# Optimization experiments

Hardware: AMD Instinct MI355X
Metric: run time of the kernel (lower is better)

The kernel has to match this reference:

```python
import jax, jax.numpy as jnp
import numpy as np

BETA = 0.85
THR = 1.0
SLOPE = 25.0  # fast_sigmoid surrogate slope

@jax.custom_vjp
def spike_fn(v):
    # Heaviside fire with fast-sigmoid surrogate gradient (snntorch fast_sigmoid)
    return (v > 0).astype(v.dtype)

def _spike_fwd(v):
    return (v > 0).astype(v.dtype), v

def _spike_bwd(v, g):
    return (g / (SLOPE * jnp.abs(v) + 1.0) ** 2,)

spike_fn.defvjp(_spike_fwd, _spike_bwd)

def setup_inputs() -> dict:
    key = jax.random.key(0)
    k1, k2, k3, k4, k5 = jax.random.split(key, 5)
    B, T, IN, H = 32, 2048, 512, 256
    x = jax.random.normal(k1, (B, T, IN), dtype=jnp.float32)
    s_in = 1.0 / np.sqrt(IN)
    s_h = 1.0 / np.sqrt(H)
    W_in = jax.random.uniform(k2, (H, IN), jnp.float32, -s_in, s_in)
    b_in = jax.random.uniform(k3, (H,), jnp.float32, -s_in, s_in)
    V = jax.random.uniform(k4, (H, H), jnp.float32, -s_h, s_h)   # RLeaky recurrent linear
    b_rec = jax.random.uniform(k5, (H,), jnp.float32, -s_h, s_h)
    return {"x": x, "W_in": W_in, "b_in": b_in, "V": V, "b_rec": b_rec}

def reference(x, W_in, b_in, V, b_rec):
    B, T, _ = x.shape
    H = W_in.shape[0]
    # input projection for all timesteps at once: (B,T,H) -> (T,B,H)
    proj = jnp.einsum('bti,hi->bth', x, W_in) + b_in
    proj_t = jnp.transpose(proj, (1, 0, 2))

    def step(carry, p_t):
        spk, mem = carry
        input_ = p_t + spk                       # combined = proj[:,t] + spk
        rec = spk @ V.T + b_rec                   # RLeaky recurrent term
        reset = jax.lax.stop_gradient((mem > THR).astype(mem.dtype))
        mem = BETA * mem + input_ + rec - reset * THR  # subtract reset
        spk = spike_fn(mem - THR)
        return (spk, mem), spk

    init = (jnp.zeros((B, H), x.dtype), jnp.zeros((B, H), x.dtype))
    _, spikes = jax.lax.scan(step, init, proj_t)  # (T,B,H)
    return jnp.transpose(spikes, (1, 0, 2))       # (B,T,H)
```

## Files before the change

### kernel.cpp

```cpp
#include <hip/hip_runtime.h>
#include <cstddef>
#include <cstdint>

#define kB 32
#define kT 2048
#define kIn 512
#define kH 256
#define kBeta 0.85f
#define kThr 1.0f

#define N_SCAN kB
#define N_GEMM (kB * 8)
#define FLAGS_PER_B 8

#define GBM 256
#define GBK 16
#define GLDA 260

#define SSTRIDE 260
#define SM_PBUF 16
#define SM_PRING (SM_PBUF + 16 * SSTRIDE)
#define SM_OBUF  (SM_PRING + 16 * 256)
#define SMEM_SCAN (SM_OBUF + 8 * 256)
#define SMEM_GEMM (2 * GBK * GLDA)
#define SMEM_FLOATS (SMEM_SCAN > SMEM_GEMM ? SMEM_SCAN : SMEM_GEMM)

__device__ __forceinline__ void wait_flag(int* f) {
    while (__hip_atomic_load(f, __ATOMIC_ACQUIRE, __HIP_MEMORY_SCOPE_AGENT) == 0) {
        __builtin_amdgcn_s_sleep(2);
    }
}

__device__ __forceinline__ void scan_bar() {
    asm volatile("s_waitcnt lgkmcnt(0)" ::: "memory");
    __builtin_amdgcn_s_barrier();
}

__device__ void gemm_body(const float* __restrict__ A,
                          const float* __restrict__ W,
                          const float* __restrict__ bias,
                          float* __restrict__ P,
                          int* flags, int gid, float* smem)
{
    float* As = smem;
    float* Bs = smem + GBK * GLDA;
    const int tid = threadIdx.x;
    const int b  = gid & 31;
    const int tt = gid >> 5;
    const int bm = b * kT + tt * GBM;
    const int tx = tid & 31;
    const int ty = tid >> 5;

    float acc[8][8];
#pragma unroll
    for (int i = 0; i < 8; ++i)
#pragma unroll
        for (int j = 0; j < 8; ++j) acc[i][j] = 0.f;

    const int r = tid >> 2, kc = (tid & 3) << 2;

    for (int kb = 0; kb < kIn; kb += GBK) {
        const float4 av = *reinterpret_cast<const float4*>(A + (size_t)(bm + r) * kIn + kb + kc);
        const float4 bv = *reinterpret_cast<const float4*>(W + (size_t)r * kIn + kb + kc);
        __syncthreads();
        As[(kc + 0) * GLDA + r] = av.x;
        As[(kc + 1) * GLDA + r] = av.y;
        As[(kc + 2) * GLDA + r] = av.z;
        As[(kc + 3) * GLDA + r] = av.w;
        Bs[(kc + 0) * GLDA + r] = bv.x;
        Bs[(kc + 1) * GLDA + r] = bv.y;
        Bs[(kc + 2) * GLDA + r] = bv.z;
        Bs[(kc + 3) * GLDA + r] = bv.w;
        __syncthreads();

#pragma unroll
        for (int k = 0; k < GBK; ++k) {
            const float4 aa0 = *reinterpret_cast<const float4*>(&As[k * GLDA + ty * 4]);
            const float4 aa1 = *reinterpret_cast<const float4*>(&As[k * GLDA + ty * 4 + 128]);
            const float4 bb0 = *reinterpret_cast<const float4*>(&Bs[k * GLDA + tx * 4]);
            const float4 bb1 = *reinterpret_cast<const float4*>(&Bs[k * GLDA + tx * 4 + 128]);
            const float av8[8] = {aa0.x, aa0.y, aa0.z, aa0.w, aa1.x, aa1.y, aa1.z, aa1.w};
            const float bv8[8] = {bb0.x, bb0.y, bb0.z, bb0.w, bb1.x, bb1.y, bb1.z, bb1.w};
#pragma unroll
            for (int i = 0; i < 8; ++i)
#pragma unroll
                for (int j = 0; j < 8; ++j)
                    acc[i][j] = fmaf(av8[i], bv8[j], acc[i][j]);
        }
    }

    const float4 bl = *reinterpret_cast<const float4*>(bias + tx * 4);
    const float4 bh = *reinterpret_cast<const float4*>(bias + tx * 4 + 128);
#pragma unroll
    for (int i = 0; i < 8; ++i) {
        const int m = bm + ty * 4 + (i & 3) + ((i >> 2) << 7);
        float4 o0, o1;
        o0.x = acc[i][0] + bl.x; o0.y = acc[i][1] + bl.y;
        o0.z = acc[i][2] + bl.z; o0.w = acc[i][3] + bl.w;
        o1.x = acc[i][4] + bh.x; o1.y = acc[i][5] + bh.y;
        o1.z = acc[i][6] + bh.z; o1.w = acc[i][7] + bh.w;
        *reinterpret_cast<float4*>(P + (size_t)m * kH + tx * 4) = o0;
        *reinterpret_cast<float4*>(P + (size_t)m * kH + tx * 4 + 128) = o1;
    }

    __syncthreads();
    if (flags && tid == 0) {
        __threadfence();
        atomicAdd(flags + b * FLAGS_PER_B + tt, 1);
    }
}

__device__ void scan_body(float* __restrict__ PO,
                          const float* __restrict__ V,
                          const float* __restrict__ brec,
                          int* flags, float* smem)
{
    unsigned long long* smask = reinterpret_cast<unsigned long long*>(smem);
    float* pbuf  = smem + SM_PBUF;
    float* pring = smem + SM_PRING;
    float* obuf  = smem + SM_OBUF;

    const int b = blockIdx.x;
    const int tid = threadIdx.x;
    const int w = tid >> 6;
    const int l = tid & 63;
    const int h0 = l << 2;
    const int kc = w << 4;
    const bool owner = (tid < kH);
    const int h = tid & (kH - 1);

    float Vr[4][16];
#pragma unroll
    for (int i = 0; i < 4; ++i) {
        const float4* vp = reinterpret_cast<const float4*>(V + (size_t)(h0 + i) * kH + kc);
#pragma unroll
        for (int c4 = 0; c4 < 4; ++c4) {
            const float4 v = vp[c4];
            Vr[i][c4 * 4 + 0] = v.x; Vr[i][c4 * 4 + 1] = v.y;
            Vr[i][c4 * 4 + 2] = v.z; Vr[i][c4 * 4 + 3] = v.w;
        }
    }

    const float br = owner ? brec[h] : 0.f;
    float mem = 0.f, spk = 0.f;
    float* po_b = PO + (size_t)b * (size_t)kT * kH;

    if (tid < 4) smask[tid] = 0ull;

    int* bflags = flags ? (flags + b * FLAGS_PER_B) : nullptr;

    if (w == 15) {
        if (bflags) wait_flag(bflags + 0);
#pragma unroll
        for (int r = 0; r < 8; ++r) {
            const float4 v = *reinterpret_cast<const float4*>(po_b + (size_t)r * kH + 4 * l);
            *reinterpret_cast<float4*>(pring + r * 256 + 4 * l) = v;
        }
    }
    scan_bar();

    const int mshift = (w & 3) << 4;

    for (int tb = 0; tb < kT / 8; ++tb) {
        float4 g0, g1, g2, g3, g4, g5, g6, g7;
#pragma unroll
        for (int ti = 0; ti < 8; ++ti) {
            const int t = tb * 8 + ti;

            if (ti == 0) {
                if (w == 15 && tb < kT / 8 - 1) {
                    if (bflags && ((tb + 1) & 31) == 0 && ((tb + 1) >> 5) < 8)
                        wait_flag(bflags + ((tb + 1) >> 5));
                    const size_t r0 = (size_t)(tb * 8 + 8) * kH + 4 * l;
                    g0 = *reinterpret_cast<const float4*>(po_b + r0 + 0 * kH);
                    g1 = *reinterpret_cast<const float4*>(po_b + r0 + 1 * kH);
                    g2 = *reinterpret_cast<const float4*>(po_b + r0 + 2 * kH);
                    g3 = *reinterpret_cast<const float4*>(po_b + r0 + 3 * kH);
                    g4 = *reinterpret_cast<const float4*>(po_b + r0 + 4 * kH);
                    g5 = *reinterpret_cast<const float4*>(po_b + r0 + 5 * kH);
                    g6 = *reinterpret_cast<const float4*>(po_b + r0 + 6 * kH);
                    g7 = *reinterpret_cast<const float4*>(po_b + r0 + 7 * kH);
                }
                if (w == 14 && tb > 0) {
#pragma unroll
                    for (int r = 0; r < 8; ++r) {
                        const float4 v = *reinterpret_cast<const float4*>(obuf + r * 256 + 4 * l);
                        *reinterpret_cast<float4*>(po_b + (size_t)((tb - 1) * 8 + r) * kH + 4 * l) = v;
                    }
                }
            }
            if (ti == 2 && w == 15 && tb < kT / 8 - 1) {
                const int s0 = (tb & 1) ? 0 : 8;
                *reinterpret_cast<float4*>(pring + (s0 + 0) * 256 + 4 * l) = g0;
                *reinterpret_cast<float4*>(pring + (s0 + 1) * 256 + 4 * l) = g1;
                *reinterpret_cast<float4*>(pring + (s0 + 2) * 256 + 4 * l) = g2;
                *reinterpret_cast<float4*>(pring + (s0 + 3) * 256 + 4 * l) = g3;
                *reinterpret_cast<float4*>(pring + (s0 + 4) * 256 + 4 * l) = g4;
                *reinterpret_cast<float4*>(pring + (s0 + 5) * 256 + 4 * l) = g5;
                *reinterpret_cast<float4*>(pring + (s0 + 6) * 256 + 4 * l) = g6;
                *reinterpret_cast<float4*>(pring + (s0 + 7) * 256 + 4 * l) = g7;
            }

            float pld = 0.f;
            if (owner) pld = pring[(t & 15) * 256 + h];

            const unsigned long long m = smask[w >> 2];
            const uint32_t chunk =
                __builtin_amdgcn_readfirstlane((uint32_t)(m >> mshift)) & 0xFFFFu;

            float a0 = 0.f, a1 = 0.f, a2 = 0.f, a3 = 0.f;
#pragma unroll
            for (int n = 0; n < 4; ++n) {
                const uint32_t nib = (chunk >> (n * 4)) & 0xFu;
                if (nib) {
#pragma unroll
                    for (int bit = 0; bit < 4; ++bit) {
                        const int j = n * 4 + bit;
                        const float bf = (float)((nib >> bit) & 1u);
                        a0 = fmaf(bf, Vr[0][j], a0);
                        a1 = fmaf(bf, Vr[1][j], a1);
                        a2 = fmaf(bf, Vr[2][j], a2);
                        a3 = fmaf(bf, Vr[3][j], a3);
                    }
                }
            }
            float4 part; part.x = a0; part.y = a1; part.z = a2; part.w = a3;
            *reinterpret_cast<float4*>(pbuf + w * SSTRIDE + h0) = part;

            scan_bar();

            if (owner) {
                float s0  = pbuf[ 0 * SSTRIDE + h], s1  = pbuf[ 1 * SSTRIDE + h];
                float s2  = pbuf[ 2 * SSTRIDE + h], s3  = pbuf[ 3 * SSTRIDE + h];
                float s4  = pbuf[ 4 * SSTRIDE + h], s5  = pbuf[ 5 * SSTRIDE + h];
                float s6  = pbuf[ 6 * SSTRIDE + h], s7  = pbuf[ 7 * SSTRIDE + h];
                float s8  = pbuf[ 8 * SSTRIDE + h], s9  = pbuf[ 9 * SSTRIDE + h];
                float s10 = pbuf[10 * SSTRIDE + h], s11 = pbuf[11 * SSTRIDE + h];
                float s12 = pbuf[12 * SSTRIDE + h], s13 = pbuf[13 * SSTRIDE + h];
                float s14 = pbuf[14 * SSTRIDE + h], s15 = pbuf[15 * SSTRIDE + h];
                const float r0 = (s0 + s1) + (s2 + s3);
                const float r1 = (s4 + s5) + (s6 + s7);
                const float r2 = (s8 + s9) + (s10 + s11);
                const float r3 = (s12 + s13) + (s14 + s15);
                const float rec = ((r0 + r1) + (r2 + r3)) + br;
                const float p = pld;
                float m2;
                {
#pragma clang fp contract(off)
                    const float input_ = p + spk;
                    m2 = kBeta * mem;
                    m2 = m2 + input_;
                    m2 = m2 + rec;
                    m2 = m2 - spk * kThr;
                }
                const bool fire = (m2 > kThr);
                const float ns = fire ? 1.0f : 0.0f;
                const unsigned long long bm = __ballot(fire);
                if ((tid & 63) == 0) smask[tid >> 6] = bm;
                obuf[ti * 256 + h] = ns;
                mem = m2;
                spk = ns;
            }

            scan_bar();
        }
    }

    if (w == 14) {
#pragma unroll
        for (int r = 0; r < 8; ++r) {
            const float4 v = *reinterpret_cast<const float4*>(obuf + r * 256 + 4 * l);
            *reinterpret_cast<float4*>(po_b + (size_t)((kT / 8 - 1) * 8 + r) * kH + 4 * l) = v;
        }
    }
}

__global__ void __launch_bounds__(1024, 4)
fused(const float* __restrict__ x, const float* __restrict__ W,
      const float* __restrict__ b_in, const float* __restrict__ V,
      const float* __restrict__ b_rec, float* __restrict__ PO,
      int* flags, int n_scan)
{
    __shared__ __align__(16) float smem[SMEM_FLOATS];
    if ((int)blockIdx.x < n_scan) {
        scan_body(PO, V, b_rec, flags, smem);
    } else {
        gemm_body(x, W, b_in, PO, flags, (int)blockIdx.x - n_scan, smem);
    }
}

extern "C" void kernel_launch(void* const* d_in, const int* in_sizes, int n_in,
                              void* d_out, int out_size, void* d_ws, size_t ws_size,
                              hipStream_t stream) {
    const float* x     = (const float*)d_in[0];
    const float* W_in  = (const float*)d_in[1];
    const float* b_in  = (const float*)d_in[2];
    const float* V     = (const float*)d_in[3];
    const float* b_rec = (const float*)d_in[4];
    float* out = (float*)d_out;

    const size_t flag_bytes = (size_t)N_SCAN * FLAGS_PER_B * sizeof(int);
    if (ws_size >= flag_bytes) {
        int* flags = (int*)d_ws;
        hipMemsetAsync(flags, 0, flag_bytes, stream);
        fused<<<N_SCAN + N_GEMM, 1024, 0, stream>>>(x, W_in, b_in, V, b_rec,
                                                    out, flags, N_SCAN);
    } else {
        fused<<<N_GEMM, 1024, 0, stream>>>(x, W_in, b_in, V, b_rec, out, nullptr, 0);
        fused<<<N_SCAN, 1024, 0, stream>>>(x, W_in, b_in, V, b_rec, out, nullptr, N_SCAN);
    }
}
```

Before: 1.804 ms.

## Spread scan epilogue across all waves with swizzle reduction and byte spike mask

```diff
diff --git a/kernel.cpp b/kernel.cpp
--- a/kernel.cpp
+++ b/kernel.cpp
@@ -12,13 +12,15 @@
 #define N_SCAN kB
 #define N_GEMM (kB * 8)
 #define FLAGS_PER_B 8
+#define NTB (kT / 8)
 
 #define GBM 256
 #define GBK 16
 #define GLDA 260
 
 #define SSTRIDE 260
-#define SM_PBUF 16
+#define SM_SBYTE_F 0
+#define SM_PBUF  128
 #define SM_PRING (SM_PBUF + 16 * SSTRIDE)
 #define SM_OBUF  (SM_PRING + 16 * 256)
 #define SMEM_SCAN (SM_OBUF + 8 * 256)
@@ -34,6 +36,13 @@
 __device__ __forceinline__ void scan_bar() {
     asm volatile("s_waitcnt lgkmcnt(0)" ::: "memory");
     __builtin_amdgcn_s_barrier();
+}
+
+__device__ __forceinline__ float swz_xor1(float x) {
+    return __int_as_float(__builtin_amdgcn_ds_swizzle(__float_as_int(x), 0x041F));
+}
+__device__ __forceinline__ float swz_xor2(float x) {
+    return __int_as_float(__builtin_amdgcn_ds_swizzle(__float_as_int(x), 0x081F));
 }
 
 __device__ void gemm_body(const float* __restrict__ A,
@@ -115,7 +124,7 @@
                           const float* __restrict__ brec,
                           int* flags, float* smem)
 {
-    unsigned long long* smask = reinterpret_cast<unsigned long long*>(smem);
+    uint8_t* sbyte = reinterpret_cast<uint8_t*>(smem + SM_SBYTE_F);
     float* pbuf  = smem + SM_PBUF;
     float* pring = smem + SM_PRING;
     float* obuf  = smem + SM_OBUF;
@@ -126,8 +135,8 @@
     const int l = tid & 63;
     const int h0 = l << 2;
     const int kc = w << 4;
-    const bool owner = (tid < kH);
-    const int h = tid & (kH - 1);
+    const int sub = l & 3;
+    const int myh = (w << 4) + (l >> 2);
 
     float Vr[4][16];
 #pragma unroll
@@ -141,137 +150,97 @@
         }
     }
 
-    const float br = owner ? brec[h] : 0.f;
+    const float br = brec[myh];
     float mem = 0.f, spk = 0.f;
     float* po_b = PO + (size_t)b * (size_t)kT * kH;
 
-    if (tid < 4) smask[tid] = 0ull;
+    if (tid < 128) reinterpret_cast<uint32_t*>(sbyte)[tid] = 0u;
 
     int* bflags = flags ? (flags + b * FLAGS_PER_B) : nullptr;
 
-    if (w == 15) {
-        if (bflags) wait_flag(bflags + 0);
-#pragma unroll
-        for (int r = 0; r < 8; ++r) {
-            const float4 v = *reinterpret_cast<const float4*>(po_b + (size_t)r * kH + 4 * l);
-            *reinterpret_cast<float4*>(pring + r * 256 + 4 * l) = v;
-        }
+    if (bflags) wait_flag(bflags + 0);
+    {
+        const float2 iv = *reinterpret_cast<const float2*>(po_b + 2 * tid);
+        *reinterpret_cast<float2*>(pring + 2 * tid) = iv;
     }
     scan_bar();
 
-    const int mshift = (w & 3) << 4;
-
-    for (int tb = 0; tb < kT / 8; ++tb) {
-        float4 g0, g1, g2, g3, g4, g5, g6, g7;
+    for (int tb = 0; tb < NTB; ++tb) {
+        float2 gld;
 #pragma unroll
         for (int ti = 0; ti < 8; ++ti) {
             const int t = tb * 8 + ti;
 
             if (ti == 0) {
-                if (w == 15 && tb < kT / 8 - 1) {
-                    if (bflags && ((tb + 1) & 31) == 0 && ((tb + 1) >> 5) < 8)
+                if (tb > 0) {
+                    const float2 d = *reinterpret_cast<const float2*>(obuf + 2 * tid);
+                    *reinterpret_cast<float2*>(po_b + (size_t)(tb - 1) * 2048 + 2 * tid) = d;
+                }
+                if (tb < NTB - 1) {
+                    if (bflags && ((tb + 1) & 31) == 0)
                         wait_flag(bflags + ((tb + 1) >> 5));
-                    const size_t r0 = (size_t)(tb * 8 + 8) * kH + 4 * l;
-                    g0 = *reinterpret_cast<const float4*>(po_b + r0 + 0 * kH);
-                    g1 = *reinterpret_cast<const float4*>(po_b + r0 + 1 * kH);
-                    g2 = *reinterpret_cast<const float4*>(po_b + r0 + 2 * kH);
-                    g3 = *reinterpret_cast<const float4*>(po_b + r0 + 3 * kH);
-                    g4 = *reinterpret_cast<const float4*>(po_b + r0 + 4 * kH);
-                    g5 = *reinterpret_cast<const float4*>(po_b + r0 + 5 * kH);
-                    g6 = *reinterpret_cast<const float4*>(po_b + r0 + 6 * kH);
-                    g7 = *reinterpret_cast<const float4*>(po_b + r0 + 7 * kH);
+                    gld = *reinterpret_cast<const float2*>(po_b + (size_t)(tb + 1) * 2048 + 2 * tid);
                 }
-                if (w == 14 && tb > 0) {
-#pragma unroll
-                    for (int r = 0; r < 8; ++r) {
-                        const float4 v = *reinterpret_cast<const float4*>(obuf + r * 256 + 4 * l);
-                        *reinterpret_cast<float4*>(po_b + (size_t)((tb - 1) * 8 + r) * kH + 4 * l) = v;
-                    }
-                }
-            }
-            if (ti == 2 && w == 15 && tb < kT / 8 - 1) {
+            }
+            if (ti == 6 && tb < NTB - 1) {
                 const int s0 = (tb & 1) ? 0 : 8;
-                *reinterpret_cast<float4*>(pring + (s0 + 0) * 256 + 4 * l) = g0;
-                *reinterpret_cast<float4*>(pring + (s0 + 1) * 256 + 4 * l) = g1;
-                *reinterpret_cast<float4*>(pring + (s0 + 2) * 256 + 4 * l) = g2;
-                *reinterpret_cast<float4*>(pring + (s0 + 3) * 256 + 4 * l) = g3;
-                *reinterpret_cast<float4*>(pring + (s0 + 4) * 256 + 4 * l) = g4;
-                *reinterpret_cast<float4*>(pring + (s0 + 5) * 256 + 4 * l) = g5;
-                *reinterpret_cast<float4*>(pring + (s0 + 6) * 256 + 4 * l) = g6;
-                *reinterpret_cast<float4*>(pring + (s0 + 7) * 256 + 4 * l) = g7;
-            }
-
-            float pld = 0.f;
-            if (owner) pld = pring[(t & 15) * 256 + h];
-
-            const unsigned long long m = smask[w >> 2];
-            const uint32_t chunk =
-                __builtin_amdgcn_readfirstlane((uint32_t)(m >> mshift)) & 0xFFFFu;
-
+                *reinterpret_cast<float2*>(pring + s0 * 256 + 2 * tid) = gld;
+            }
+
+            const float pld = pring[((t & 15) << 8) + myh];
+
+            const uint4 cw = *reinterpret_cast<const uint4*>(
+                sbyte + ((t & 1) << 8) + (w << 4));
+            const uint32_t cws[4] = {cw.x, cw.y, cw.z, cw.w};
             float a0 = 0.f, a1 = 0.f, a2 = 0.f, a3 = 0.f;
 #pragma unroll
-            for (int n = 0; n < 4; ++n) {
-                const uint32_t nib = (chunk >> (n * 4)) & 0xFu;
-                if (nib) {
-#pragma unroll
-                    for (int bit = 0; bit < 4; ++bit) {
-                        const int j = n * 4 + bit;
-                        const float bf = (float)((nib >> bit) & 1u);
-                        a0 = fmaf(bf, Vr[0][j], a0);
-                        a1 = fmaf(bf, Vr[1][j], a1);
-                        a2 = fmaf(bf, Vr[2][j], a2);
-                        a3 = fmaf(bf, Vr[3][j], a3);
-                    }
-                }
+            for (int j = 0; j < 16; ++j) {
+                const float bf = (float)((cws[j >> 2] >> ((j & 3) * 8)) & 0xFFu);
+                a0 = fmaf(bf, Vr[0][j], a0);
+                a1 = fmaf(bf, Vr[1][j], a1);
+                a2 = fmaf(bf, Vr[2][j], a2);
+                a3 = fmaf(bf, Vr[3][j], a3);
             }
             float4 part; part.x = a0; part.y = a1; part.z = a2; part.w = a3;
             *reinterpret_cast<float4*>(pbuf + w * SSTRIDE + h0) = part;
 
             scan_bar();
 
-            if (owner) {
-                float s0  = pbuf[ 0 * SSTRIDE + h], s1  = pbuf[ 1 * SSTRIDE + h];
-                float s2  = pbuf[ 2 * SSTRIDE + h], s3  = pbuf[ 3 * SSTRIDE + h];
-                float s4  = pbuf[ 4 * SSTRIDE + h], s5  = pbuf[ 5 * SSTRIDE + h];
-                float s6  = pbuf[ 6 * SSTRIDE + h], s7  = pbuf[ 7 * SSTRIDE + h];
-                float s8  = pbuf[ 8 * SSTRIDE + h], s9  = pbuf[ 9 * SSTRIDE + h];
-                float s10 = pbuf[10 * SSTRIDE + h], s11 = pbuf[11 * SSTRIDE + h];
-                float s12 = pbuf[12 * SSTRIDE + h], s13 = pbuf[13 * SSTRIDE + h];
-                float s14 = pbuf[14 * SSTRIDE + h], s15 = pbuf[15 * SSTRIDE + h];
-                const float r0 = (s0 + s1) + (s2 + s3);
-                const float r1 = (s4 + s5) + (s6 + s7);
-                const float r2 = (s8 + s9) + (s10 + s11);
-                const float r3 = (s12 + s13) + (s14 + s15);
-                const float rec = ((r0 + r1) + (r2 + r3)) + br;
-                const float p = pld;
-                float m2;
-                {
+            const float pp0 = pbuf[(4 * sub + 0) * SSTRIDE + myh];
+            const float pp1 = pbuf[(4 * sub + 1) * SSTRIDE + myh];
+            const float pp2 = pbuf[(4 * sub + 2) * SSTRIDE + myh];
+            const float pp3 = pbuf[(4 * sub + 3) * SSTRIDE + myh];
+            const float rsub = (pp0 + pp1) + (pp2 + pp3);
+            const float u    = rsub + swz_xor1(rsub);
+            const float rec0 = u + swz_xor2(u);
+            const float rec  = rec0 + br;
+
+            const float p = pld;
+            float m2;
+            {
 #pragma clang fp contract(off)
-                    const float input_ = p + spk;
-                    m2 = kBeta * mem;
-                    m2 = m2 + input_;
-                    m2 = m2 + rec;
-                    m2 = m2 - spk * kThr;
-                }
-                const bool fire = (m2 > kThr);
-                const float ns = fire ? 1.0f : 0.0f;
-                const unsigned long long bm = __ballot(fire);
-                if ((tid & 63) == 0) smask[tid >> 6] = bm;
-                obuf[ti * 256 + h] = ns;
-                mem = m2;
-                spk = ns;
-            }
+                const float input_ = p + spk;
+                m2 = kBeta * mem;
+                m2 = m2 + input_;
+                m2 = m2 + rec;
+                m2 = m2 - spk * kThr;
+            }
+            const bool fire = (m2 > kThr);
+            const float ns = fire ? 1.0f : 0.0f;
+            if (sub == 0) {
+                obuf[(ti << 8) + myh] = ns;
+                sbyte[(((t & 1) ^ 1) << 8) + myh] = fire ? 1 : 0;
+            }
+            mem = m2;
+            spk = ns;
 
             scan_bar();
         }
     }
 
-    if (w == 14) {
-#pragma unroll
-        for (int r = 0; r < 8; ++r) {
-            const float4 v = *reinterpret_cast<const float4*>(obuf + r * 256 + 4 * l);
-            *reinterpret_cast<float4*>(po_b + (size_t)((kT / 8 - 1) * 8 + r) * kH + 4 * l) = v;
-        }
+    {
+        const float2 d = *reinterpret_cast<const float2*>(obuf + 2 * tid);
+        *reinterpret_cast<float2*>(po_b + (size_t)(NTB - 1) * 2048 + 2 * tid) = d;
     }
 }
 
```

Measured after the change: 1.960 ms. +8.7%, slower.
